# Performance work log

Measured on AMD Instinct MI355X. Metric: run time of the kernel, lower is better.

The kernel has to match this reference:

```python
import jax, jax.numpy as jnp
import numpy as np

B, S, D, H = 2, 2048, 2048, 16
HD = D // H  # 128
MAX_POS = 2048


def make_sinusoidal_positions(num_pos, dim):
    inv_freq = 1.0 / 10000 ** (np.arange(0, dim, 2) / dim)
    freqs = np.einsum('i,j->ij', np.arange(num_pos), inv_freq).astype('float32')
    emb = np.concatenate((freqs, freqs), axis=-1)  # (num_pos, dim)
    out = np.concatenate((np.sin(emb)[:, None, :], np.cos(emb)[:, None, :]), axis=-1)  # (num_pos,1,2*dim)
    return jnp.array(out[:, :, :num_pos])  # slice is a no-op since num_pos >= 2*dim


_SINCOS = make_sinusoidal_positions(MAX_POS, HD)


def rotate_half(x):
    return jnp.concatenate((-x[..., x.shape[-1] // 2:], x[..., :x.shape[-1] // 2]), axis=-1)


def setup_inputs() -> dict:
    key = jax.random.key(0)
    ks = jax.random.split(key, 5)
    std = 0.02
    return {
        'hidden_states': jax.random.normal(ks[0], (B, S, D), jnp.float32),
        'attention_mask': jnp.ones((B, S), jnp.int32),
        'position_ids': jnp.broadcast_to(jnp.arange(S, dtype=jnp.int32), (B, S)),
        'Wq': jax.random.normal(ks[1], (D, D), jnp.float32) * std,
        'Wk': jax.random.normal(ks[2], (D, D), jnp.float32) * std,
        'Wv': jax.random.normal(ks[3], (D, D), jnp.float32) * std,
        'Wo': jax.random.normal(ks[4], (D, D), jnp.float32) * std,
    }


def reference(hidden_states, attention_mask, position_ids, Wq, Wk, Wv, Wo):
    b, s, d = hidden_states.shape
    # QKV projections, split heads -> (b, s, H, HD)
    q = (hidden_states @ Wq).reshape(b, s, H, HD)
    k = (hidden_states @ Wk).reshape(b, s, H, HD)
    v = (hidden_states @ Wv).reshape(b, s, H, HD)
    # RoPE: embed_positions[position_ids] -> (b, s, 1, 2*HD); split -> sin, cos (b,s,1,HD)
    sincos = _SINCOS[position_ids]
    sin_pos, cos_pos = jnp.split(sincos, 2, axis=-1)
    q = q * cos_pos + rotate_half(q) * sin_pos
    k = k * cos_pos + rotate_half(k) * sin_pos
    # causal + padding mask -> additive bias
    causal = jnp.tril(jnp.ones((s, s), dtype=bool))  # (q, k)
    mask = (attention_mask[:, None, None, :] > 0) & causal[None, None, :, :]  # (b,1,s,s)
    bias = jnp.where(mask, jnp.float32(0.0), jnp.finfo(q.dtype).min).astype(q.dtype)
    # dot_product_attention_weights: scale query, scores + bias, softmax
    scale = jnp.asarray(1.0 / np.sqrt(HD), q.dtype)
    scores = jnp.einsum('bqhd,bkhd->bhqk', q * scale, k) + bias
    attn = jax.nn.softmax(scores, axis=-1)
    out = jnp.einsum('bhqk,bkhd->bqhd', attn, v).reshape(b, s, d)
    return out @ Wo
```

## Files before the change

### kernel.cpp

```cpp
#include <hip/hip_runtime.h>
#include <stdint.h>
#include <math.h>

#define BATCH 2
#define SEQ 2048
#define DM 2048
#define NH 16
#define HD 128

typedef unsigned short u16;
typedef __attribute__((ext_vector_type(8))) __bf16 bf16x8;
typedef __attribute__((ext_vector_type(8))) _Float16 f16x8;
typedef __attribute__((ext_vector_type(4))) float f32x4;
typedef __attribute__((ext_vector_type(4))) unsigned short u16x4;

__device__ inline float bf2f(u16 x) {
    return __uint_as_float(((unsigned)x) << 16);
}
__device__ inline u16 f2bf(float f) {
    unsigned u = __float_as_uint(f);
    return (u16)((u + 0x7FFF + ((u >> 16) & 1)) >> 16);
}
__device__ inline u16 f2h(float f) {
    union { _Float16 h; u16 u; } c;
    c.h = (_Float16)f;
    return c.u;
}
__device__ inline f32x4 mfma16(bf16x8 a, bf16x8 b, f32x4 c) {
    return __builtin_amdgcn_mfma_f32_16x16x32_bf16(a, b, c, 0, 0, 0);
}
__device__ inline f32x4 mfma16h(f16x8 a, f16x8 b, f32x4 c) {
    return __builtin_amdgcn_mfma_f32_16x16x32_f16(a, b, c, 0, 0, 0);
}
__device__ inline void cp16(const u16* g, u16* l) {
    __builtin_amdgcn_global_load_lds(
        (const __attribute__((address_space(1))) unsigned int*)g,
        (__attribute__((address_space(3))) unsigned int*)l, 16, 0, 0);
}

__global__ __launch_bounds__(256) void transpose2048(const float* __restrict__ src,
                                                     u16* __restrict__ dst) {
    __shared__ u16 tile[32][33];
    int bx = blockIdx.x * 32, by = blockIdx.y * 32;
    int tx = threadIdx.x & 31, ty = threadIdx.x >> 5;
    #pragma unroll
    for (int i = 0; i < 32; i += 8)
        tile[ty + i][tx] = f2bf(src[(long)(by + ty + i) * DM + bx + tx]);
    __syncthreads();
    #pragma unroll
    for (int i = 0; i < 32; i += 8)
        dst[(long)(bx + ty + i) * DM + by + tx] = tile[tx][ty + i];
}

__global__ __launch_bounds__(256) void xcast(const float* __restrict__ X,
                                             u16* __restrict__ Xb) {
    long i = ((long)blockIdx.x * 256 + threadIdx.x) * 8;
    float4 v0 = *(const float4*)&X[i];
    float4 v1 = *(const float4*)&X[i + 4];
    union { uint4 q; u16 e[8]; } u;
    u.e[0] = f2bf(v0.x); u.e[1] = f2bf(v0.y);
    u.e[2] = f2bf(v0.z); u.e[3] = f2bf(v0.w);
    u.e[4] = f2bf(v1.x); u.e[5] = f2bf(v1.y);
    u.e[6] = f2bf(v1.z); u.e[7] = f2bf(v1.w);
    *(uint4*)&Xb[i] = u.q;
}

#define BM 128
#define BN 128
#define BK 64

template <bool OUTF32, bool VTRANS>
__global__ __launch_bounds__(256) void gemm_bt(const u16* __restrict__ A,
                                               const u16* __restrict__ Bt,
                                               void* __restrict__ Cv,
                                               int N, int K) {
    __shared__ alignas(16) u16 As[BM * BK];
    __shared__ alignas(16) u16 Bs[BN * BK];
    int tid = threadIdx.x;
    int wave = tid >> 6, lane = tid & 63;
    int quad = lane >> 4, l16 = lane & 15;
    int wm = wave & 1, wn = wave >> 1;
    long rowBase = (long)blockIdx.y * BM;
    long colBase = (long)blockIdx.x * BN;

    f32x4 acc[4][4];
    #pragma unroll
    for (int i = 0; i < 4; i++)
        #pragma unroll
        for (int j = 0; j < 4; j++) acc[i][j] = (f32x4){0.f, 0.f, 0.f, 0.f};

    for (int k0 = 0; k0 < K; k0 += BK) {
        #pragma unroll
        for (int p = 0; p < 4; p++) {
            int idx = (p << 8) + tid;
            int r = idx >> 3, c8 = (idx & 7) << 3;
            cp16(&A[(rowBase + r) * K + k0 + c8], &As[idx << 3]);
            cp16(&Bt[(colBase + r) * K + k0 + c8], &Bs[idx << 3]);
        }
        __syncthreads();
        #pragma unroll
        for (int kk = 0; kk < 2; kk++) {
            bf16x8 af[4], bfr[4];
            #pragma unroll
            for (int i = 0; i < 4; i++)
                af[i] = *(const bf16x8*)&As[(wm * 64 + i * 16 + l16) * 64 + kk * 32 + quad * 8];
            #pragma unroll
            for (int j = 0; j < 4; j++)
                bfr[j] = *(const bf16x8*)&Bs[(wn * 64 + j * 16 + l16) * 64 + kk * 32 + quad * 8];
            #pragma unroll
            for (int i = 0; i < 4; i++)
                #pragma unroll
                for (int j = 0; j < 4; j++)
                    acc[i][j] = mfma16(af[i], bfr[j], acc[i][j]);
        }
        __syncthreads();
    }
    #pragma unroll
    for (int i = 0; i < 4; i++) {
        #pragma unroll
        for (int j = 0; j < 4; j++) {
            long col = colBase + wn * 64 + j * 16 + l16;
            if (VTRANS) {
                long row0 = rowBase + wm * 64 + i * 16 + quad * 4;
                long bb = row0 >> 11, ss = row0 & (SEQ - 1);
                long hh = col >> 7, dd = col & (HD - 1);
                u16x4 pk;
                #pragma unroll
                for (int r = 0; r < 4; r++) pk[r] = f2h(acc[i][j][r]);
                *(u16x4*)&((u16*)Cv)[(((bb * NH) + hh) * HD + dd) * SEQ + ss] = pk;
            } else {
                #pragma unroll
                for (int r = 0; r < 4; r++) {
                    long row = rowBase + wm * 64 + i * 16 + quad * 4 + r;
                    if (OUTF32) ((float*)Cv)[row * N + col] = acc[i][j][r];
                    else        ((u16*)Cv)[row * N + col] = f2bf(acc[i][j][r]);
                }
            }
        }
    }
}

__global__ __launch_bounds__(256) void rope_kernel(u16* __restrict__ Q,
                                                   u16* __restrict__ Kb,
                                                   const int* __restrict__ pid) {
    int idx = blockIdx.x * blockDim.x + threadIdx.x;
    int d = idx & 63;
    int h = (idx >> 6) & (NH - 1);
    int m = idx >> 10;
    int b = m >> 11, s = m & (SEQ - 1);
    int pos = pid[b * SEQ + s];
    float invf = __builtin_amdgcn_exp2f(-(float)d * 0.20762050593046015f);
    float freq = (float)pos * invf;
    float sn = __sinf(freq);
    float cs = __cosf(freq);
    long base = (long)m * DM + h * HD + d;
    float x1 = bf2f(Q[base]), x2 = bf2f(Q[base + 64]);
    Q[base] = f2bf(x1 * cs - x2 * sn);
    Q[base + 64] = f2bf(x2 * cs + x1 * sn);
    float y1 = bf2f(Kb[base]), y2 = bf2f(Kb[base + 64]);
    Kb[base] = f2bf(y1 * cs - y2 * sn);
    Kb[base + 64] = f2bf(y2 * cs + y1 * sn);
}

__global__ __launch_bounds__(64) void attn_mfma(const u16* __restrict__ Q,
                                                const u16* __restrict__ K,
                                                const u16* __restrict__ Vt,
                                                const int* __restrict__ amask,
                                                u16* __restrict__ O) {
    __shared__ alignas(16) u16 Pw[32 * 72];
    int lane = threadIdx.x;
    int quad = lane >> 4, l16 = lane & 15;
    int bh = blockIdx.x;
    int qblk = gridDim.y - 1 - blockIdx.y;
    int b = bh >> 4, h = bh & (NH - 1);
    int qbase = qblk * 32;
    long head = (long)b * SEQ * DM + (long)h * HD;
    const u16* Vh = Vt + (long)bh * HD * SEQ;
    const int* mrow = amask + b * SEQ;

    bf16x8 qf[2][4];
    #pragma unroll
    for (int i = 0; i < 2; i++)
        #pragma unroll
        for (int kk = 0; kk < 4; kk++)
            qf[i][kk] = *(const bf16x8*)&Q[head + (long)(qbase + i * 16 + l16) * DM + kk * 32 + quad * 8];

    f32x4 of[2][8];
    #pragma unroll
    for (int i = 0; i < 2; i++)
        #pragma unroll
        for (int j = 0; j < 8; j++) of[i][j] = (f32x4){0.f, 0.f, 0.f, 0.f};
    float lsum[2][4] = {{0.f, 0.f, 0.f, 0.f}, {0.f, 0.f, 0.f, 0.f}};
    const float k2 = 0.12752792143808157f;
    const float C2 = 7.213475204444817f;

    int ntiles = (qbase + 32 + 63) >> 6;
    for (int t = 0; t < ntiles; t++) {
        int kv0 = t << 6;
        bf16x8 kf[16];
        #pragma unroll
        for (int half = 0; half < 4; half++)
            #pragma unroll
            for (int kk = 0; kk < 4; kk++)
                kf[half * 4 + kk] = *(const bf16x8*)&K[head + (long)(kv0 + half * 16 + l16) * DM + kk * 32 + quad * 8];
        int am[4];
        #pragma unroll
        for (int half = 0; half < 4; half++) am[half] = mrow[kv0 + half * 16 + l16];
        f32x4 sacc[2][4];
        #pragma unroll
        for (int i = 0; i < 2; i++)
            #pragma unroll
            for (int half = 0; half < 4; half++) sacc[i][half] = (f32x4){0.f, 0.f, 0.f, 0.f};
        #pragma unroll
        for (int half = 0; half < 4; half++)
            #pragma unroll
            for (int kk = 0; kk < 4; kk++) {
                sacc[0][half] = mfma16(qf[0][kk], kf[half * 4 + kk], sacc[0][half]);
                sacc[1][half] = mfma16(qf[1][kk], kf[half * 4 + kk], sacc[1][half]);
            }
        f16x8 vf[16];
        #pragma unroll
        for (int c = 0; c < 2; c++)
            #pragma unroll
            for (int j = 0; j < 8; j++)
                vf[c * 8 + j] = *(const f16x8*)&Vh[(long)(j * 16 + l16) * SEQ + kv0 + c * 32 + quad * 8];
        #pragma unroll
        for (int i = 0; i < 2; i++)
            #pragma unroll
            for (int half = 0; half < 4; half++) {
                int kvc = kv0 + half * 16 + l16;
                #pragma unroll
                for (int r = 0; r < 4; r++) {
                    int qr = qbase + i * 16 + quad * 4 + r;
                    float p = (kvc <= qr && am[half] > 0)
                                  ? __builtin_amdgcn_exp2f(sacc[i][half][r] * k2 - C2) : 0.f;
                    lsum[i][r] += p;
                    Pw[(i * 16 + quad * 4 + r) * 72 + half * 16 + l16] = f2h(p);
                }
            }
        f16x8 pf[2][2];
        #pragma unroll
        for (int i = 0; i < 2; i++)
            #pragma unroll
            for (int c = 0; c < 2; c++)
                pf[i][c] = *(const f16x8*)&Pw[(i * 16 + l16) * 72 + c * 32 + quad * 8];
        #pragma unroll
        for (int c = 0; c < 2; c++)
            #pragma unroll
            for (int j = 0; j < 8; j++) {
                of[0][j] = mfma16h(pf[0][c], vf[c * 8 + j], of[0][j]);
                of[1][j] = mfma16h(pf[1][c], vf[c * 8 + j], of[1][j]);
            }
    }
    #pragma unroll
    for (int i = 0; i < 2; i++) {
        float inv[4];
        #pragma unroll
        for (int r = 0; r < 4; r++) {
            float s = lsum[i][r];
            s += __shfl_xor(s, 1, 64);
            s += __shfl_xor(s, 2, 64);
            s += __shfl_xor(s, 4, 64);
            s += __shfl_xor(s, 8, 64);
            inv[r] = 1.0f / s;
        }
        #pragma unroll
        for (int j = 0; j < 8; j++)
            #pragma unroll
            for (int r = 0; r < 4; r++)
                O[head + (long)(qbase + i * 16 + quad * 4 + r) * DM + j * 16 + l16] =
                    f2bf(of[i][j][r] * inv[r]);
    }
}

extern "C" void kernel_launch(void* const* d_in, const int* in_sizes, int n_in,
                              void* d_out, int out_size, void* d_ws, size_t ws_size,
                              hipStream_t stream) {
    const float* X  = (const float*)d_in[0];
    const int* am   = (const int*)d_in[1];
    const int* pid  = (const int*)d_in[2];
    const float* Wq = (const float*)d_in[3];
    const float* Wk = (const float*)d_in[4];
    const float* Wv = (const float*)d_in[5];
    const float* Wo = (const float*)d_in[6];
    float* out = (float*)d_out;

    char* ws = (char*)d_ws;
    const size_t MB = 1024 * 1024;
    u16* WoT = (u16*)(ws + 0 * MB);
    u16* WqT = (u16*)(ws + 8 * MB);
    u16* WkT = (u16*)(ws + 16 * MB);
    u16* WvT = (u16*)(ws + 24 * MB);
    u16* Qb  = (u16*)(ws + 32 * MB);
    u16* Kb  = (u16*)(ws + 48 * MB);
    u16* Vt  = (u16*)(ws + 8 * MB);
    u16* Xb  = (u16*)d_out;

    dim3 tb(256);
    dim3 tg(64, 64);
    transpose2048<<<tg, tb, 0, stream>>>(Wq, WqT);
    transpose2048<<<tg, tb, 0, stream>>>(Wk, WkT);
    transpose2048<<<tg, tb, 0, stream>>>(Wv, WvT);
    transpose2048<<<tg, tb, 0, stream>>>(Wo, WoT);
    xcast<<<(BATCH * SEQ * DM) / (256 * 8), tb, 0, stream>>>(X, Xb);

    dim3 gg(DM / BN, (BATCH * SEQ) / BM);
    gemm_bt<false, false><<<gg, tb, 0, stream>>>(Xb, WqT, Qb, DM, DM);
    gemm_bt<false, false><<<gg, tb, 0, stream>>>(Xb, WkT, Kb, DM, DM);
    gemm_bt<false, true ><<<gg, tb, 0, stream>>>(Xb, WvT, Vt, DM, DM);

    int nrope = BATCH * SEQ * NH * 64;
    rope_kernel<<<nrope / 256, tb, 0, stream>>>(Qb, Kb, pid);

    dim3 ag(BATCH * NH, SEQ / 32);
    attn_mfma<<<ag, dim3(64), 0, stream>>>(Qb, Kb, Vt, am, Qb);

    gemm_bt<true, false><<<gg, tb, 0, stream>>>(Qb, WoT, out, DM, DM);
}
```

Before: 502.9 us.

## Split attention KV tiles across two waves; fuse QKV GEMM and weight transposes

```diff
diff --git a/kernel.cpp b/kernel.cpp
--- a/kernel.cpp
+++ b/kernel.cpp
@@ -38,9 +38,22 @@
         (__attribute__((address_space(3))) unsigned int*)l, 16, 0, 0);
 }
 
-__global__ __launch_bounds__(256) void transpose2048(const float* __restrict__ src,
-                                                     u16* __restrict__ dst) {
+__global__ __launch_bounds__(256) void transpose4(const float* __restrict__ s0,
+                                                  const float* __restrict__ s1,
+                                                  const float* __restrict__ s2,
+                                                  const float* __restrict__ s3,
+                                                  u16* __restrict__ d0,
+                                                  u16* __restrict__ d1,
+                                                  u16* __restrict__ d2,
+                                                  u16* __restrict__ d3) {
     __shared__ u16 tile[32][33];
+    const float* src; u16* dst;
+    switch (blockIdx.z) {
+        case 0: src = s0; dst = d0; break;
+        case 1: src = s1; dst = d1; break;
+        case 2: src = s2; dst = d2; break;
+        default: src = s3; dst = d3; break;
+    }
     int bx = blockIdx.x * 32, by = blockIdx.y * 32;
     int tx = threadIdx.x & 31, ty = threadIdx.x >> 5;
     #pragma unroll
@@ -69,11 +82,82 @@
 #define BN 128
 #define BK 64
 
-template <bool OUTF32, bool VTRANS>
-__global__ __launch_bounds__(256) void gemm_bt(const u16* __restrict__ A,
-                                               const u16* __restrict__ Bt,
-                                               void* __restrict__ Cv,
-                                               int N, int K) {
+__global__ __launch_bounds__(256) void gemm_qkv(const u16* __restrict__ A,
+                                                const u16* __restrict__ Wcat,
+                                                u16* __restrict__ Qb,
+                                                u16* __restrict__ Kb,
+                                                u16* __restrict__ Vt) {
+    __shared__ alignas(16) u16 As[BM * BK];
+    __shared__ alignas(16) u16 Bs[BN * BK];
+    int tid = threadIdx.x;
+    int wave = tid >> 6, lane = tid & 63;
+    int quad = lane >> 4, l16 = lane & 15;
+    int wm = wave & 1, wn = wave >> 1;
+    long rowBase = (long)blockIdx.y * BM;
+    long colG = (long)blockIdx.x * BN;
+    int mat = (int)(colG >> 11);
+    long colBase = colG & (DM - 1);
+
+    f32x4 acc[4][4];
+    #pragma unroll
+    for (int i = 0; i < 4; i++)
+        #pragma unroll
+        for (int j = 0; j < 4; j++) acc[i][j] = (f32x4){0.f, 0.f, 0.f, 0.f};
+
+    for (int k0 = 0; k0 < DM; k0 += BK) {
+        #pragma unroll
+        for (int p = 0; p < 4; p++) {
+            int idx = (p << 8) + tid;
+            int r = idx >> 3, c8 = (idx & 7) << 3;
+            cp16(&A[(rowBase + r) * DM + k0 + c8], &As[idx << 3]);
+            cp16(&Wcat[(colG + r) * DM + k0 + c8], &Bs[idx << 3]);
+        }
+        __syncthreads();
+        #pragma unroll
+        for (int kk = 0; kk < 2; kk++) {
+            bf16x8 af[4], bfr[4];
+            #pragma unroll
+            for (int i = 0; i < 4; i++)
+                af[i] = *(const bf16x8*)&As[(wm * 64 + i * 16 + l16) * 64 + kk * 32 + quad * 8];
+            #pragma unroll
+            for (int j = 0; j < 4; j++)
+                bfr[j] = *(const bf16x8*)&Bs[(wn * 64 + j * 16 + l16) * 64 + kk * 32 + quad * 8];
+            #pragma unroll
+            for (int i = 0; i < 4; i++)
+                #pragma unroll
+                for (int j = 0; j < 4; j++)
+                    acc[i][j] = mfma16(af[i], bfr[j], acc[i][j]);
+        }
+        __syncthreads();
+    }
+    #pragma unroll
+    for (int i = 0; i < 4; i++) {
+        #pragma unroll
+        for (int j = 0; j < 4; j++) {
+            long col = colBase + wn * 64 + j * 16 + l16;
+            if (mat == 2) {
+                long row0 = rowBase + wm * 64 + i * 16 + quad * 4;
+                long bb = row0 >> 11, ss = row0 & (SEQ - 1);
+                long hh = col >> 7, dd = col & (HD - 1);
+                u16x4 pk;
+                #pragma unroll
+                for (int r = 0; r < 4; r++) pk[r] = f2h(acc[i][j][r]);
+                *(u16x4*)&Vt[(((bb * NH) + hh) * HD + dd) * SEQ + ss] = pk;
+            } else {
+                u16* C = (mat == 0) ? Qb : Kb;
+                #pragma unroll
+                for (int r = 0; r < 4; r++) {
+                    long row = rowBase + wm * 64 + i * 16 + quad * 4 + r;
+                    C[row * DM + col] = f2bf(acc[i][j][r]);
+                }
+            }
+        }
+    }
+}
+
+__global__ __launch_bounds__(256) void gemm_out(const u16* __restrict__ A,
+                                                const u16* __restrict__ Bt,
+                                                float* __restrict__ C) {
     __shared__ alignas(16) u16 As[BM * BK];
     __shared__ alignas(16) u16 Bs[BN * BK];
     int tid = threadIdx.x;
@@ -89,13 +173,13 @@
         #pragma unroll
         for (int j = 0; j < 4; j++) acc[i][j] = (f32x4){0.f, 0.f, 0.f, 0.f};
 
-    for (int k0 = 0; k0 < K; k0 += BK) {
+    for (int k0 = 0; k0 < DM; k0 += BK) {
         #pragma unroll
         for (int p = 0; p < 4; p++) {
             int idx = (p << 8) + tid;
             int r = idx >> 3, c8 = (idx & 7) << 3;
-            cp16(&A[(rowBase + r) * K + k0 + c8], &As[idx << 3]);
-            cp16(&Bt[(colBase + r) * K + k0 + c8], &Bs[idx << 3]);
+            cp16(&A[(rowBase + r) * DM + k0 + c8], &As[idx << 3]);
+            cp16(&Bt[(colBase + r) * DM + k0 + c8], &Bs[idx << 3]);
         }
         __syncthreads();
         #pragma unroll
@@ -116,28 +200,16 @@
         __syncthreads();
     }
     #pragma unroll
-    for (int i = 0; i < 4; i++) {
+    for (int i = 0; i < 4; i++)
         #pragma unroll
         for (int j = 0; j < 4; j++) {
             long col = colBase + wn * 64 + j * 16 + l16;
-            if (VTRANS) {
-                long row0 = rowBase + wm * 64 + i * 16 + quad * 4;
-                long bb = row0 >> 11, ss = row0 & (SEQ - 1);
-                long hh = col >> 7, dd = col & (HD - 1);
-                u16x4 pk;
-                #pragma unroll
-                for (int r = 0; r < 4; r++) pk[r] = f2h(acc[i][j][r]);
-                *(u16x4*)&((u16*)Cv)[(((bb * NH) + hh) * HD + dd) * SEQ + ss] = pk;
-            } else {
-                #pragma unroll
-                for (int r = 0; r < 4; r++) {
-                    long row = rowBase + wm * 64 + i * 16 + quad * 4 + r;
-                    if (OUTF32) ((float*)Cv)[row * N + col] = acc[i][j][r];
-                    else        ((u16*)Cv)[row * N + col] = f2bf(acc[i][j][r]);
-                }
-            }
-        }
-    }
+            #pragma unroll
+            for (int r = 0; r < 4; r++) {
+                long row = rowBase + wm * 64 + i * 16 + quad * 4 + r;
+                C[row * DM + col] = acc[i][j][r];
+            }
+        }
 }
 
 __global__ __launch_bounds__(256) void rope_kernel(u16* __restrict__ Q,
@@ -162,13 +234,14 @@
     Kb[base + 64] = f2bf(y2 * cs + y1 * sn);
 }
 
-__global__ __launch_bounds__(64) void attn_mfma(const u16* __restrict__ Q,
-                                                const u16* __restrict__ K,
-                                                const u16* __restrict__ Vt,
-                                                const int* __restrict__ amask,
-                                                u16* __restrict__ O) {
-    __shared__ alignas(16) u16 Pw[32 * 72];
-    int lane = threadIdx.x;
+__global__ __launch_bounds__(128, 4) void attn_mfma(const u16* __restrict__ Q,
+                                                    const u16* __restrict__ K,
+                                                    const u16* __restrict__ Vt,
+                                                    const int* __restrict__ amask,
+                                                    u16* __restrict__ O) {
+    __shared__ alignas(16) char smem[19456];
+    int tid = threadIdx.x;
+    int w = tid >> 6, lane = tid & 63;
     int quad = lane >> 4, l16 = lane & 15;
     int bh = blockIdx.x;
     int qblk = gridDim.y - 1 - blockIdx.y;
@@ -177,13 +250,7 @@
     long head = (long)b * SEQ * DM + (long)h * HD;
     const u16* Vh = Vt + (long)bh * HD * SEQ;
     const int* mrow = amask + b * SEQ;
-
-    bf16x8 qf[2][4];
-    #pragma unroll
-    for (int i = 0; i < 2; i++)
-        #pragma unroll
-        for (int kk = 0; kk < 4; kk++)
-            qf[i][kk] = *(const bf16x8*)&Q[head + (long)(qbase + i * 16 + l16) * DM + kk * 32 + quad * 8];
+    u16* Pw = (u16*)smem + w * (32 * 72);
 
     f32x4 of[2][8];
     #pragma unroll
@@ -195,8 +262,14 @@
     const float C2 = 7.213475204444817f;
 
     int ntiles = (qbase + 32 + 63) >> 6;
-    for (int t = 0; t < ntiles; t++) {
+    for (int t = w; t < ntiles; t += 2) {
         int kv0 = t << 6;
+        bf16x8 qf[2][4];
+        #pragma unroll
+        for (int i = 0; i < 2; i++)
+            #pragma unroll
+            for (int kk = 0; kk < 4; kk++)
+                qf[i][kk] = *(const bf16x8*)&Q[head + (long)(qbase + i * 16 + l16) * DM + kk * 32 + quad * 8];
         bf16x8 kf[16];
         #pragma unroll
         for (int half = 0; half < 4; half++)
@@ -218,12 +291,6 @@
                 sacc[0][half] = mfma16(qf[0][kk], kf[half * 4 + kk], sacc[0][half]);
                 sacc[1][half] = mfma16(qf[1][kk], kf[half * 4 + kk], sacc[1][half]);
             }
-        f16x8 vf[16];
-        #pragma unroll
-        for (int c = 0; c < 2; c++)
-            #pragma unroll
-            for (int j = 0; j < 8; j++)
-                vf[c * 8 + j] = *(const f16x8*)&Vh[(long)(j * 16 + l16) * SEQ + kv0 + c * 32 + quad * 8];
         #pragma unroll
         for (int i = 0; i < 2; i++)
             #pragma unroll
@@ -248,28 +315,57 @@
         for (int c = 0; c < 2; c++)
             #pragma unroll
             for (int j = 0; j < 8; j++) {
-                of[0][j] = mfma16h(pf[0][c], vf[c * 8 + j], of[0][j]);
-                of[1][j] = mfma16h(pf[1][c], vf[c * 8 + j], of[1][j]);
-            }
-    }
-    #pragma unroll
-    for (int i = 0; i < 2; i++) {
-        float inv[4];
-        #pragma unroll
-        for (int r = 0; r < 4; r++) {
-            float s = lsum[i][r];
-            s += __shfl_xor(s, 1, 64);
-            s += __shfl_xor(s, 2, 64);
-            s += __shfl_xor(s, 4, 64);
-            s += __shfl_xor(s, 8, 64);
-            inv[r] = 1.0f / s;
-        }
-        #pragma unroll
-        for (int j = 0; j < 8; j++)
-            #pragma unroll
-            for (int r = 0; r < 4; r++)
-                O[head + (long)(qbase + i * 16 + quad * 4 + r) * DM + j * 16 + l16] =
-                    f2bf(of[i][j][r] * inv[r]);
+                f16x8 vf = *(const f16x8*)&Vh[(long)(j * 16 + l16) * SEQ + kv0 + c * 32 + quad * 8];
+                of[0][j] = mfma16h(pf[0][c], vf, of[0][j]);
+                of[1][j] = mfma16h(pf[1][c], vf, of[1][j]);
+            }
+    }
+    __syncthreads();
+    float* of_lds = (float*)smem;
+    float* ls_lds = (float*)(smem + 17408);
+    if (w == 1) {
+        #pragma unroll
+        for (int i = 0; i < 2; i++)
+            #pragma unroll
+            for (int j = 0; j < 8; j++)
+                *(f32x4*)&of_lds[lane * 68 + (i * 8 + j) * 4] = of[i][j];
+        #pragma unroll
+        for (int i = 0; i < 2; i++)
+            #pragma unroll
+            for (int r = 0; r < 4; r++) ls_lds[lane * 8 + i * 4 + r] = lsum[i][r];
+    }
+    __syncthreads();
+    if (w == 0) {
+        #pragma unroll
+        for (int i = 0; i < 2; i++)
+            #pragma unroll
+            for (int j = 0; j < 8; j++) {
+                f32x4 v = *(const f32x4*)&of_lds[lane * 68 + (i * 8 + j) * 4];
+                of[i][j] += v;
+            }
+        #pragma unroll
+        for (int i = 0; i < 2; i++)
+            #pragma unroll
+            for (int r = 0; r < 4; r++) lsum[i][r] += ls_lds[lane * 8 + i * 4 + r];
+        #pragma unroll
+        for (int i = 0; i < 2; i++) {
+            float inv[4];
+            #pragma unroll
+            for (int r = 0; r < 4; r++) {
+                float s = lsum[i][r];
+                s += __shfl_xor(s, 1, 64);
+                s += __shfl_xor(s, 2, 64);
+                s += __shfl_xor(s, 4, 64);
+                s += __shfl_xor(s, 8, 64);
+                inv[r] = 1.0f / s;
+            }
+            #pragma unroll
+            for (int j = 0; j < 8; j++)
+                #pragma unroll
+                for (int r = 0; r < 4; r++)
+                    O[head + (long)(qbase + i * 16 + quad * 4 + r) * DM + j * 16 + l16] =
+                        f2bf(of[i][j][r] * inv[r]);
+        }
     }
 }
 
@@ -293,27 +389,20 @@
     u16* WvT = (u16*)(ws + 24 * MB);
     u16* Qb  = (u16*)(ws + 32 * MB);
     u16* Kb  = (u16*)(ws + 48 * MB);
-    u16* Vt  = (u16*)(ws + 8 * MB);
     u16* Xb  = (u16*)d_out;
+    u16* Vt  = (u16*)((char*)d_out + 16 * MB);
 
     dim3 tb(256);
-    dim3 tg(64, 64);
-    transpose2048<<<tg, tb, 0, stream>>>(Wq, WqT);
-    transpose2048<<<tg, tb, 0, stream>>>(Wk, WkT);
-    transpose2048<<<tg, tb, 0, stream>>>(Wv, WvT);
-    transpose2048<<<tg, tb, 0, stream>>>(Wo, WoT);
+    transpose4<<<dim3(64, 64, 4), tb, 0, stream>>>(Wq, Wk, Wv, Wo, WqT, WkT, WvT, WoT);
     xcast<<<(BATCH * SEQ * DM) / (256 * 8), tb, 0, stream>>>(X, Xb);
 
-    dim3 gg(DM / BN, (BATCH * SEQ) / BM);
-    gemm_bt<false, false><<<gg, tb, 0, stream>>>(Xb, WqT, Qb, DM, DM);
-    gemm_bt<false, false><<<gg, tb, 0, stream>>>(Xb, WkT, Kb, DM, DM);
-    gemm_bt<false, true ><<<gg, tb, 0, stream>>>(Xb, WvT, Vt, DM, DM);
+    gemm_qkv<<<dim3(3 * DM / BN, (BATCH * SEQ) / BM), tb, 0, stream>>>(Xb, WqT, Qb, Kb, Vt);
 
     int nrope = BATCH * SEQ * NH * 64;
     rope_kernel<<<nrope / 256, tb, 0, stream>>>(Qb, Kb, pid);
 
     dim3 ag(BATCH * NH, SEQ / 32);
-    attn_mfma<<<ag, dim3(64), 0, stream>>>(Qb, Kb, Vt, am, Qb);
-
-    gemm_bt<true, false><<<gg, tb, 0, stream>>>(Qb, WoT, out, DM, DM);
-}
+    attn_mfma<<<ag, dim3(128), 0, stream>>>(Qb, Kb, Vt, am, Qb);
+
+    gemm_out<<<dim3(DM / BN, (BATCH * SEQ) / BM), tb, 0, stream>>>(Qb, WoT, out);
+}
```

New measurement: 662.6 us. +31.8%, slower.
